# Kernel optimization log

Measured on AMD Instinct MI355X. Metric: run time of the kernel, lower is better.

## Reference

```python
import jax, jax.numpy as jnp
import numpy as np

N_NODES = 50000
N_EDGES = 800000
DIM_IN = 64
DIM_HID = 128
DIM_OUT = 64


def _linear_init(key, fan_in, fan_out):
    # torch nn.Linear default: U(-1/sqrt(fan_in), 1/sqrt(fan_in)) for W and b
    kw, kb = jax.random.split(key)
    bound = 1.0 / np.sqrt(fan_in)
    W = jax.random.uniform(kw, (fan_in, fan_out), minval=-bound, maxval=bound, dtype=jnp.float32)
    b = jax.random.uniform(kb, (fan_out,), minval=-bound, maxval=bound, dtype=jnp.float32)
    return W, b


def setup_inputs() -> dict:
    key = jax.random.key(0)
    kx, ke, k0, k1, k2 = jax.random.split(key, 5)
    x = jax.random.normal(kx, (N_NODES, DIM_IN), dtype=jnp.float32)
    edge_idx = jax.random.randint(ke, (2, N_EDGES), 0, N_NODES, dtype=jnp.int64)
    W0, b0 = _linear_init(k0, 2 * DIM_IN, DIM_HID)
    W1, b1 = _linear_init(k1, DIM_HID, DIM_HID)
    W2, b2 = _linear_init(k2, DIM_HID, DIM_OUT)
    return {"x": x, "edge_idx": edge_idx, "W0": W0, "b0": b0,
            "W1": W1, "b1": b1, "W2": W2, "b2": b2}


def reference(x, edge_idx, W0, b0, W1, b1, W2, b2):
    row, col = edge_idx[0], edge_idx[1]
    # gather + concat edge features: [E, 2*dim_in]
    h = jnp.concatenate([x[row], x[col]], axis=-1)
    h = jax.nn.softplus(h @ W0 + b0)
    h = jax.nn.softplus(h @ W1 + b1)
    h = h @ W2 + b2  # [E, dim_out]
    # scatter-add edge messages to source nodes
    return jax.ops.segment_sum(h, row, num_segments=x.shape[0])
```

## Files before the change

kernel.cpp:

```cpp
#include <hip/hip_runtime.h>
#include <math.h>

#define N_NODES 50000
#define N_EDGES 800000
#define DIM_IN 64
#define DIM_HID 128
#define DIM_OUT 64
#define PAD 136

typedef __attribute__((ext_vector_type(8))) short short8;
typedef __attribute__((ext_vector_type(4))) float f32x4;

union U8 { uint4 u; short8 s; };

__device__ __forceinline__ unsigned short f2bf(float f) {
    unsigned u = __float_as_uint(f);
    return (unsigned short)((u + 0x7fffu + ((u >> 16) & 1u)) >> 16);
}

__device__ __forceinline__ unsigned cvt_pk_bf16(float a, float b) {
#if __has_builtin(__builtin_amdgcn_cvt_pk_bf16_f32)
    auto pk = __builtin_amdgcn_cvt_pk_bf16_f32(a, b);
    unsigned d; __builtin_memcpy(&d, &pk, 4);
    return d;
#else
    return (unsigned)f2bf(a) | ((unsigned)f2bf(b) << 16);
#endif
}

__device__ __forceinline__ float exp2_fast(float a) {
#if __has_builtin(__builtin_amdgcn_exp2f)
    return __builtin_amdgcn_exp2f(a);
#else
    return __expf(a * 0.69314718f);
#endif
}

__device__ __forceinline__ unsigned sp2(float x0, float x1) {
    const float L2E = 1.44269504f;
    float z0 = exp2_fast(-fabsf(x0) * L2E);
    float z1 = exp2_fast(-fabsf(x1) * L2E);
    float p0 = fmaf(fmaf(fmaf(-0.1011458f, z0, 0.2942925f), z0, -0.5f), z0, 1.0f) * z0;
    float p1 = fmaf(fmaf(fmaf(-0.1011458f, z1, 0.2942925f), z1, -0.5f), z1, 1.0f) * z1;
    return cvt_pk_bf16(fmaxf(x0, 0.0f) + p0, fmaxf(x1, 0.0f) + p1);
}

__global__ void prep_weights(const float* __restrict__ W0,
                             const float* __restrict__ W1,
                             const float* __restrict__ W2,
                             unsigned short* __restrict__ wt) {
    int i = blockIdx.x * blockDim.x + threadIdx.x;
    if (i >= 320 * PAD) return;
    int row = i / PAD, s = i - row * PAD;
    float v = 0.f;
    if (s < 128) {
        int f = ((s >> 5) << 5) | (((s & 7) >> 2) << 4) | (((s >> 3) & 3) << 2) | (s & 3);
        if (row < 128)      v = W0[s * DIM_HID + row];
        else if (row < 256) v = W1[f * DIM_HID + (row - 128)];
        else                v = W2[f * DIM_OUT + (row - 256)];
    }
    wt[i] = f2bf(v);
}

__global__ __launch_bounds__(256, 4)
void edge_mlp_mfma(const float* __restrict__ x,
                   const int* __restrict__ eidx,
                   const unsigned short* __restrict__ wt,
                   const float* __restrict__ b0,
                   const float* __restrict__ b1,
                   const float* __restrict__ b2,
                   float* __restrict__ out) {
    const int lane = threadIdx.x & 63;
    const int w    = threadIdx.x >> 6;
    const int l16  = lane & 15;
    const int q    = lane >> 4;
    const int e0w  = blockIdx.x * 128 + w * 32;

    const unsigned short* Wt0 = wt;
    const unsigned short* Wt1 = wt + 128 * PAD;
    const unsigned short* Wt2 = wt + 256 * PAD;

    int nodeR[2], nodeC[2];
#pragma unroll
    for (int m = 0; m < 2; ++m) {
        nodeR[m] = eidx[e0w + m * 16 + l16];
        nodeC[m] = eidx[N_EDGES + e0w + m * 16 + l16];
    }

    short8 hfr[2][4];
#pragma unroll
    for (int m = 0; m < 2; ++m)
#pragma unroll
        for (int kk = 0; kk < 4; ++kk) {
            int node = (kk >= 2) ? nodeC[m] : nodeR[m];
            const float* p = x + (size_t)node * DIM_IN + (kk & 1) * 32 + q * 8;
            float4 v0 = *(const float4*)p;
            float4 v1 = *(const float4*)(p + 4);
            U8 t;
            t.u.x = cvt_pk_bf16(v0.x, v0.y);
            t.u.y = cvt_pk_bf16(v0.z, v0.w);
            t.u.z = cvt_pk_bf16(v1.x, v1.y);
            t.u.w = cvt_pk_bf16(v1.z, v1.w);
            hfr[m][kk] = t.s;
        }

#pragma unroll
    for (int L = 0; L < 2; ++L) {
        const unsigned short* W = L ? Wt1 : Wt0;
        const float* bias = L ? b1 : b0;
        unsigned d[2][8][2];
#pragma unroll
        for (int ti = 0; ti < 8; ++ti) {
            f32x4 bb = *(const f32x4*)(bias + ti * 16 + q * 4);
            f32x4 a0 = bb, a1 = bb;
            const unsigned short* Wp = W + (ti * 16 + l16) * PAD + q * 8;
            short8 wf[4];
#pragma unroll
            for (int kk = 0; kk < 4; ++kk)
                wf[kk] = *(const short8*)(Wp + kk * 32);
#pragma unroll
            for (int kk = 0; kk < 4; ++kk) {
                a0 = __builtin_amdgcn_mfma_f32_16x16x32_bf16(wf[kk], hfr[0][kk], a0, 0, 0, 0);
                a1 = __builtin_amdgcn_mfma_f32_16x16x32_bf16(wf[kk], hfr[1][kk], a1, 0, 0, 0);
            }
            d[0][ti][0] = sp2(a0[0], a0[1]);
            d[0][ti][1] = sp2(a0[2], a0[3]);
            d[1][ti][0] = sp2(a1[0], a1[1]);
            d[1][ti][1] = sp2(a1[2], a1[3]);
        }
#pragma unroll
        for (int m = 0; m < 2; ++m)
#pragma unroll
            for (int kk = 0; kk < 4; ++kk) {
                U8 t;
                t.u.x = d[m][2 * kk][0];
                t.u.y = d[m][2 * kk][1];
                t.u.z = d[m][2 * kk + 1][0];
                t.u.w = d[m][2 * kk + 1][1];
                hfr[m][kk] = t.s;
            }
    }

    int nodeO[2][4];
#pragma unroll
    for (int m = 0; m < 2; ++m)
#pragma unroll
        for (int r = 0; r < 4; ++r)
            nodeO[m][r] = eidx[e0w + m * 16 + q * 4 + r];

#pragma unroll
    for (int ti = 0; ti < 4; ++ti) {
        float bv = b2[ti * 16 + l16];
        f32x4 a0 = (f32x4){bv, bv, bv, bv};
        f32x4 a1 = a0;
        const unsigned short* Wp = Wt2 + (ti * 16 + l16) * PAD + q * 8;
        short8 wf[4];
#pragma unroll
        for (int kk = 0; kk < 4; ++kk)
            wf[kk] = *(const short8*)(Wp + kk * 32);
#pragma unroll
        for (int kk = 0; kk < 4; ++kk) {
            a0 = __builtin_amdgcn_mfma_f32_16x16x32_bf16(hfr[0][kk], wf[kk], a0, 0, 0, 0);
            a1 = __builtin_amdgcn_mfma_f32_16x16x32_bf16(hfr[1][kk], wf[kk], a1, 0, 0, 0);
        }
#pragma unroll
        for (int r = 0; r < 4; ++r) {
            atomicAdd(out + (size_t)nodeO[0][r] * DIM_OUT + ti * 16 + l16, a0[r]);
            atomicAdd(out + (size_t)nodeO[1][r] * DIM_OUT + ti * 16 + l16, a1[r]);
        }
    }
}

extern "C" void kernel_launch(void* const* d_in, const int* in_sizes, int n_in,
                              void* d_out, int out_size, void* d_ws, size_t ws_size,
                              hipStream_t stream) {
    const float* x  = (const float*)d_in[0];
    const int*   ei = (const int*)d_in[1];
    const float* W0 = (const float*)d_in[2];
    const float* b0 = (const float*)d_in[3];
    const float* W1 = (const float*)d_in[4];
    const float* b1 = (const float*)d_in[5];
    const float* W2 = (const float*)d_in[6];
    const float* b2 = (const float*)d_in[7];
    float* out = (float*)d_out;
    unsigned short* wt = (unsigned short*)d_ws;

    hipMemsetAsync(out, 0, (size_t)N_NODES * DIM_OUT * sizeof(float), stream);

    const int wn = 320 * PAD;
    prep_weights<<<(wn + 255) / 256, 256, 0, stream>>>(W0, W1, W2, wt);

    edge_mlp_mfma<<<N_EDGES / 128, 256, 0, stream>>>(x, ei, wt, b0, b1, b2, out);
}
```

Before: 294.8 us.

## Pre-convert node features to bf16 and fuse zeroing and weight prep into one kernel

A single prep kernel now zeroes the output, converts x to bf16 in workspace, and packs the weights, replacing a memset plus a separate weight kernel. The edge kernel, templated on whether the bf16 copy exists, gathers bf16 rows instead of fp32, which halves the gathered bytes per edge and drops the per-edge conversion. The bf16 conversion is also forced to an inline asm instruction. This costs an extra pass over x and needs enough workspace, with the old path kept as a fallback.

```diff
diff --git a/kernel.cpp b/kernel.cpp
--- a/kernel.cpp
+++ b/kernel.cpp
@@ -19,13 +19,9 @@
 }
 
 __device__ __forceinline__ unsigned cvt_pk_bf16(float a, float b) {
-#if __has_builtin(__builtin_amdgcn_cvt_pk_bf16_f32)
-    auto pk = __builtin_amdgcn_cvt_pk_bf16_f32(a, b);
-    unsigned d; __builtin_memcpy(&d, &pk, 4);
+    unsigned d;
+    asm("v_cvt_pk_bf16_f32 %0, %1, %2" : "=v"(d) : "v"(a), "v"(b));
     return d;
-#else
-    return (unsigned)f2bf(a) | ((unsigned)f2bf(b) << 16);
-#endif
 }
 
 __device__ __forceinline__ float exp2_fast(float a) {
@@ -43,6 +39,39 @@
     float p0 = fmaf(fmaf(fmaf(-0.1011458f, z0, 0.2942925f), z0, -0.5f), z0, 1.0f) * z0;
     float p1 = fmaf(fmaf(fmaf(-0.1011458f, z1, 0.2942925f), z1, -0.5f), z1, 1.0f) * z1;
     return cvt_pk_bf16(fmaxf(x0, 0.0f) + p0, fmaxf(x1, 0.0f) + p1);
+}
+
+__global__ void prep_all(const float* __restrict__ x,
+                         const float* __restrict__ W0,
+                         const float* __restrict__ W1,
+                         const float* __restrict__ W2,
+                         unsigned short* __restrict__ wt,
+                         unsigned short* __restrict__ xbf,
+                         float4* __restrict__ outz) {
+    int i = blockIdx.x * blockDim.x + threadIdx.x;
+
+    if (i < (N_NODES * DIM_OUT / 4))
+        outz[i] = make_float4(0.f, 0.f, 0.f, 0.f);
+
+    if (i < (N_NODES * DIM_IN / 4)) {
+        float4 v = *((const float4*)x + i);
+        uint2 p;
+        p.x = cvt_pk_bf16(v.x, v.y);
+        p.y = cvt_pk_bf16(v.z, v.w);
+        *((uint2*)xbf + i) = p;
+    }
+
+    if (i < 320 * PAD) {
+        int row = i / PAD, s = i - row * PAD;
+        float v = 0.f;
+        if (s < 128) {
+            int f = ((s >> 5) << 5) | (((s & 7) >> 2) << 4) | (((s >> 3) & 3) << 2) | (s & 3);
+            if (row < 128)      v = W0[s * DIM_HID + row];
+            else if (row < 256) v = W1[f * DIM_HID + (row - 128)];
+            else                v = W2[f * DIM_OUT + (row - 256)];
+        }
+        wt[i] = f2bf(v);
+    }
 }
 
 __global__ void prep_weights(const float* __restrict__ W0,
@@ -62,8 +91,10 @@
     wt[i] = f2bf(v);
 }
 
+template <bool XB>
 __global__ __launch_bounds__(256, 4)
 void edge_mlp_mfma(const float* __restrict__ x,
+                   const unsigned short* __restrict__ xbf,
                    const int* __restrict__ eidx,
                    const unsigned short* __restrict__ wt,
                    const float* __restrict__ b0,
@@ -93,15 +124,19 @@
 #pragma unroll
         for (int kk = 0; kk < 4; ++kk) {
             int node = (kk >= 2) ? nodeC[m] : nodeR[m];
-            const float* p = x + (size_t)node * DIM_IN + (kk & 1) * 32 + q * 8;
-            float4 v0 = *(const float4*)p;
-            float4 v1 = *(const float4*)(p + 4);
-            U8 t;
-            t.u.x = cvt_pk_bf16(v0.x, v0.y);
-            t.u.y = cvt_pk_bf16(v0.z, v0.w);
-            t.u.z = cvt_pk_bf16(v1.x, v1.y);
-            t.u.w = cvt_pk_bf16(v1.z, v1.w);
-            hfr[m][kk] = t.s;
+            if (XB) {
+                hfr[m][kk] = *(const short8*)(xbf + (size_t)node * DIM_IN + (kk & 1) * 32 + q * 8);
+            } else {
+                const float* p = x + (size_t)node * DIM_IN + (kk & 1) * 32 + q * 8;
+                float4 v0 = *(const float4*)p;
+                float4 v1 = *(const float4*)(p + 4);
+                U8 t;
+                t.u.x = cvt_pk_bf16(v0.x, v0.y);
+                t.u.y = cvt_pk_bf16(v0.z, v0.w);
+                t.u.z = cvt_pk_bf16(v1.x, v1.y);
+                t.u.w = cvt_pk_bf16(v1.z, v1.w);
+                hfr[m][kk] = t.s;
+            }
         }
 
 #pragma unroll
@@ -183,12 +218,22 @@
     const float* W2 = (const float*)d_in[6];
     const float* b2 = (const float*)d_in[7];
     float* out = (float*)d_out;
+
     unsigned short* wt = (unsigned short*)d_ws;
-
-    hipMemsetAsync(out, 0, (size_t)N_NODES * DIM_OUT * sizeof(float), stream);
-
-    const int wn = 320 * PAD;
-    prep_weights<<<(wn + 255) / 256, 256, 0, stream>>>(W0, W1, W2, wt);
-
-    edge_mlp_mfma<<<N_EDGES / 128, 256, 0, stream>>>(x, ei, wt, b0, b1, b2, out);
-}
+    const size_t WT_BYTES = (size_t)320 * PAD * sizeof(unsigned short);
+    unsigned short* xbf = (unsigned short*)((char*)d_ws + WT_BYTES);
+    const size_t need = WT_BYTES + (size_t)N_NODES * DIM_IN * sizeof(unsigned short);
+
+    if (ws_size >= need) {
+        prep_all<<<(N_NODES * DIM_IN / 4 + 255) / 256, 256, 0, stream>>>(
+            x, W0, W1, W2, wt, xbf, (float4*)out);
+        edge_mlp_mfma<true><<<N_EDGES / 128, 256, 0, stream>>>(
+            x, xbf, ei, wt, b0, b1, b2, out);
+    } else {
+        hipMemsetAsync(out, 0, (size_t)N_NODES * DIM_OUT * sizeof(float), stream);
+        const int wn = 320 * PAD;
+        prep_weights<<<(wn + 255) / 256, 256, 0, stream>>>(W0, W1, W2, wt);
+        edge_mlp_mfma<false><<<N_EDGES / 128, 256, 0, stream>>>(
+            x, nullptr, ei, wt, b0, b1, b2, out);
+    }
+}
```

Measured after the change: 274.8 us. 1.07x faster.
